# Kernel tuning notes

Measured on AMD Instinct MI355X. Metric: run time of the kernel, lower is better.

Reference implementation:

```python
import jax, jax.numpy as jnp
import numpy as np

# Static config (matches init_kwargs / input_specs)
B, P, A, D, K = 8, 1, 8, 8, 3          # batch, num_plans, action_channels, dim_qk, receptive_field
T, H, W = 32, 32, 32                   # 3D grid
PAD = K // 2
PA = P * A
PAD_VALUE = 0.0


def _pad3(t, val=PAD_VALUE):
    # pad last three (spatial) dims by PAD on each side
    return jnp.pad(t, ((0, 0), (0, 0), (PAD, PAD), (PAD, PAD), (PAD, PAD)), constant_values=val)


def _conv3d(x, w):
    # x: [B, Ci, T, H, W], w: [Co, Ci, K, K, K], VALID padding (input pre-padded)
    return jax.lax.conv_general_dilated(
        x, w, window_strides=(1, 1, 1), padding='VALID',
        dimension_numbers=('NCDHW', 'OIDHW', 'NCDHW'))


def setup_inputs() -> dict:
    key = jax.random.key(0)
    k1, k2, k3, k4 = jax.random.split(key, 4)
    s = 1.0 / np.sqrt(P * K ** 3)  # conv fan-in init scale
    return {
        'values':  jax.random.normal(k1, (B, P, T, H, W), jnp.float32),
        'rewards': jax.random.normal(k2, (B, P, T, H, W), jnp.float32),
        'w_qk':    jax.random.normal(k3, (2 * PA * D, P, K, K, K), jnp.float32) * s,
        'w_v':     jax.random.normal(k4, (PA, P, K, K, K), jnp.float32) * s,
    }


def reference(values, rewards, w_qk, w_v):
    x = values + rewards                       # [B, P, T, H, W]
    xp = _pad3(x)

    qk = _conv3d(xp, w_qk)                     # [B, 2*PA*D, T, H, W]
    q, k = jnp.split(qk, 2, axis=1)            # each [B, PA*D, T, H, W]

    # softmax value-conv weights over the flattened 3D kernel per (out, in) pair
    wv = jax.nn.softmax(w_v.reshape(PA, P, K ** 3), axis=-1).reshape(w_v.shape)
    v = _conv3d(xp, wv)                        # [B, PA, T, H, W]

    kp, vp = _pad3(k), _pad3(v)
    thw = T * H * W
    qf = q.reshape(B, PA, D, thw)              # [B, A, D, thw]

    # local 3x3x3 neighborhood attention: per kernel offset, dot q with shifted k
    # (same math as unfoldNd + einsum, without the K^3*D memory blow-up)
    sims, vns = [], []
    for dt in range(K):
        for dh in range(K):
            for dw in range(K):
                ksh = jax.lax.slice(kp, (0, 0, dt, dh, dw),
                                    (B, PA * D, dt + T, dh + H, dw + W)).reshape(B, PA, D, thw)
                sims.append(jnp.einsum('badt,badt->bat', qf, ksh))
                vns.append(jax.lax.slice(vp, (0, 0, dt, dh, dw),
                                         (B, PA, dt + T, dh + H, dw + W)).reshape(B, PA, thw))

    sim = jnp.stack(sims, axis=-1)             # [B, A, thw, K^3]
    attn = jax.nn.softmax(sim, axis=-1)
    vn = jnp.stack(vns, axis=2)                # [B, A, K^3, thw]
    q_values = jnp.einsum('batn,bant->bat', attn, vn)  # [B, A, thw]

    q_values = q_values.reshape(B, P, A, T, H, W)
    # ActionSelector with soft_maxpool=False: hard max over actions
    next_values = jnp.max(q_values, axis=2)    # [B, P, T, H, W]
    return next_values
```

## Files before the change

kernel.cpp:

```cpp
#include <hip/hip_runtime.h>
#include <hip/hip_bf16.h>

#define NB   8
#define NA   8
#define ND   8
#define NCH  64
#define GT   32
#define KREG 216
#define IMS  40

#define KACT_OFF 0
#define VP_OFF   27648
#define VSTR     592
#define QU_OFF   32384
#define POOL_SZ  40576

typedef _Float16 h2_t  __attribute__((ext_vector_type(2)));
typedef _Float16 f16x8 __attribute__((ext_vector_type(8)));
typedef float    f32x4 __attribute__((ext_vector_type(4)));

static __device__ __forceinline__ unsigned pack_h2(float a, float b) {
#if __has_builtin(__builtin_amdgcn_cvt_pkrtz)
    return __builtin_bit_cast(unsigned, __builtin_amdgcn_cvt_pkrtz(a, b));
#else
    unsigned short ha = __builtin_bit_cast(unsigned short, (_Float16)a);
    unsigned short hb = __builtin_bit_cast(unsigned short, (_Float16)b);
    return (unsigned)ha | ((unsigned)hb << 16);
#endif
}

static __device__ __forceinline__ float dot2(unsigned k, unsigned q, float c) {
#if __has_builtin(__builtin_amdgcn_fdot2)
    return __builtin_amdgcn_fdot2(__builtin_bit_cast(h2_t, k),
                                  __builtin_bit_cast(h2_t, q), c, false);
#else
    h2_t a = __builtin_bit_cast(h2_t, k), b = __builtin_bit_cast(h2_t, q);
    return c + (float)a[0] * (float)b[0] + (float)a[1] * (float)b[1];
#endif
}

__launch_bounds__(256, 4)
__global__ void avi_kernel(const float* __restrict__ values,
                           const float* __restrict__ rewards,
                           const float* __restrict__ w_qk,
                           const float* __restrict__ w_v,
                           float* __restrict__ out) {
    __shared__ __align__(16) char pool[POOL_SZ];
    float*    xS   = (float*)(pool + 0);
    _Float16* BTSl = (_Float16*)(pool + 2304);
    _Float16* imc  = (_Float16*)(pool + 13824);
    char*     qU   = pool + QU_OFF;

    const int tid  = threadIdx.x;
    const int bb   = blockIdx.x >> 9;
    const int tile = blockIdx.x & 511;
    const int tz = tile >> 6, ty = (tile >> 3) & 7, tx = tile & 7;
    const int g0z = tz * 4, g0y = ty * 4, g0x = tx * 4;
    const int base_in = bb * (GT * GT * GT);

    for (int i = tid; i < 512; i += 256) {
        int lz = i >> 6, ly = (i >> 3) & 7, lx = i & 7;
        int gz = g0z + lz - 2, gy = g0y + ly - 2, gx = g0x + lx - 2;
        float v = 0.f;
        if ((unsigned)gz < 32u && (unsigned)gy < 32u && (unsigned)gx < 32u) {
            int idx = base_in + gz * 1024 + gy * 32 + gx;
            v = values[idx] + rewards[idx];
        }
        xS[lz * 72 + ly * 9 + lx] = v;
    }
    if (tid < 144) {
        float r[28];
        r[27] = 0.f;
        if (tid < 64) {
            const float* w = w_qk + (NCH + tid) * 27;
            #pragma unroll
            for (int j = 0; j < 27; ++j) r[j] = w[j];
        } else if (tid < 72) {
            int a = tid - 64;
            float m = -1e30f;
            #pragma unroll
            for (int j = 0; j < 27; ++j) { r[j] = w_v[a * 27 + j]; m = fmaxf(m, r[j]); }
            float s = 0.f;
            #pragma unroll
            for (int j = 0; j < 27; ++j) { r[j] = __expf(r[j] - m); s += r[j]; }
            float inv = 1.f / s;
            #pragma unroll
            for (int j = 0; j < 27; ++j) r[j] *= inv;
        } else if (tid < 80) {
            #pragma unroll
            for (int j = 0; j < 27; ++j) r[j] = 0.f;
        } else {
            const float* w = w_qk + (tid - 80) * 27;
            const float L2E = 1.44269504f;
            #pragma unroll
            for (int j = 0; j < 27; ++j) r[j] = w[j] * L2E;
        }
        unsigned* dst = (unsigned*)(BTSl + tid * IMS);
        #pragma unroll
        for (int p = 0; p < 14; ++p) dst[p] = pack_h2(r[2 * p], r[2 * p + 1]);
        #pragma unroll
        for (int p = 14; p < 20; ++p) dst[p] = 0u;
    }
    __syncthreads();

    if (tid < 224) {
        unsigned rowU[16];
        if (tid < KREG) {
            int vz = tid / 36, rem = tid - vz * 36, vy = rem / 6, vx = rem - vy * 6;
            int gz = g0z + vz - 1, gy = g0y + vy - 1, gx = g0x + vx - 1;
            float mask = ((unsigned)gz < 32u && (unsigned)gy < 32u && (unsigned)gx < 32u)
                             ? 1.f : 0.f;
            float xr[27];
            #pragma unroll
            for (int t = 0; t < 27; ++t) {
                int dz = t / 9, dy = (t / 3) % 3, dx = t % 3;
                xr[t] = xS[(vz + dz) * 72 + (vy + dy) * 9 + (vx + dx)] * mask;
            }
            #pragma unroll
            for (int p = 0; p < 13; ++p) rowU[p] = pack_h2(xr[2 * p], xr[2 * p + 1]);
            rowU[13] = pack_h2(xr[26], 0.f);
            rowU[14] = rowU[15] = 0u;
        } else {
            #pragma unroll
            for (int p = 0; p < 16; ++p) rowU[p] = 0u;
        }
        int4* dst = (int4*)((char*)imc + tid * (IMS * 2));
        dst[0] = make_int4(rowU[0], rowU[1], rowU[2], rowU[3]);
        dst[1] = make_int4(rowU[4], rowU[5], rowU[6], rowU[7]);
        dst[2] = make_int4(rowU[8], rowU[9], rowU[10], rowU[11]);
        dst[3] = make_int4(rowU[12], rowU[13], rowU[14], rowU[15]);
    }

    const int lane = tid & 63;
    const int wave = tid >> 6;
    const int quad = lane >> 4;
    const int l15  = lane & 15;

    f16x8 af[9];
    #pragma unroll
    for (int mt = 0; mt < 9; ++mt)
        af[mt] = *(const f16x8*)(BTSl + (mt * 16 + l15) * IMS + quad * 8);

    __syncthreads();

    f16x8 bf[4];
    #pragma unroll
    for (int i = 0; i < 4; ++i) {
        int nt = wave + i * 4;
        if (nt < 14)
            bf[i] = *(const f16x8*)(imc + (nt * 16 + l15) * IMS + quad * 8);
    }

    __syncthreads();

    for (int i = 0; i < 4; ++i) {
        int nt = wave + i * 4;
        if (nt >= 14) break;
        int n = nt * 16 + l15;
        bool nvalid = (n < KREG);
        int vz = n / 36, rm = n - vz * 36, vy = rm / 6, vx = rm - vy * 6;
        bool ctr = ((unsigned)(vz - 1) < 4u) && ((unsigned)(vy - 1) < 4u) &&
                   ((unsigned)(vx - 1) < 4u);
        int cvox = (vz - 1) * 16 + (vy - 1) * 4 + (vx - 1);
        int kp_byte = (n * 16) ^ ((vz & 1) << 4);
        int qoff = cvox * 128 +
                   ((((quad >> 1) ^ (cvox >> 2) ^ (cvox & 3)) & 7) << 4) +
                   (quad & 1) * 8;
        #pragma unroll
        for (int mt = 0; mt < 9; ++mt) {
            f32x4 d = __builtin_amdgcn_mfma_f32_16x16x32_f16(
                af[mt], bf[i], (f32x4){0.f, 0.f, 0.f, 0.f}, 0, 0, 0);
            if (mt < 4) {
                if (nvalid) {
                    int a = mt * 2 + (quad >> 1);
                    int2 w2;
                    w2.x = (int)pack_h2(d[0], d[1]);
                    w2.y = (int)pack_h2(d[2], d[3]);
                    *(int2*)(pool + KACT_OFF + a * 3456 + kp_byte + (quad & 1) * 8) = w2;
                }
            } else if (mt == 4) {
                if (nvalid && quad < 2) {
                    #pragma unroll
                    for (int j = 0; j < 4; ++j)
                        *(_Float16*)(pool + VP_OFF + (quad * 4 + j) * VSTR +
                                     vz * 96 + vy * 16 + vx * 2) = (_Float16)d[j];
                }
            } else {
                if (ctr) {
                    int2 w2;
                    w2.x = (int)pack_h2(d[0], d[1]);
                    w2.y = (int)pack_h2(d[2], d[3]);
                    *(int2*)(qU + (qoff ^ ((mt - 5) << 5))) = w2;
                }
            }
        }
    }
    __syncthreads();

    const int a    = (tid >> 4) & 7;
    const int row  = tid & 15;
    const int h    = tid >> 7;
    const int clz2 = row >> 2, cly2 = row & 3;

    unsigned qp[4][4];
    {
        const char* qb = qU + row * 512;
        const int   u0 = (a ^ row) & 7;
        #pragma unroll
        for (int x = 0; x < 4; ++x) {
            const int4 qv = *(const int4*)(qb + x * 128 + ((u0 ^ x) << 4));
            qp[x][0] = (unsigned)qv.x; qp[x][1] = (unsigned)qv.y;
            qp[x][2] = (unsigned)qv.z; qp[x][3] = (unsigned)qv.w;
        }
    }

    float ssum[4] = {0.f, 0.f, 0.f, 0.f};
    float acc[4]  = {0.f, 0.f, 0.f, 0.f};

    const int   p   = clz2 & 1;
    const char* b0  = pool + KACT_OFF + a * 3456 + clz2 * 576 + cly2 * 96;
    const char* PAp = b0 + p * 16;
    const char* PBp = b0 + 16 - p * 16;
    const char* vb  = pool + VP_OFF + a * VSTR + clz2 * 96 + cly2 * 16;

#define STEP(PTA, PTB, KI, VI) do {                                           \
        int4 km[6];                                                           \
        km[0] = *(const int4*)((PTA) + (KI));                                 \
        km[1] = *(const int4*)((PTB) + (KI));                                 \
        km[2] = *(const int4*)((PTA) + (KI) + 32);                            \
        km[3] = *(const int4*)((PTB) + (KI) + 32);                            \
        km[4] = *(const int4*)((PTA) + (KI) + 64);                            \
        km[5] = *(const int4*)((PTB) + (KI) + 64);                            \
        f16x8 vv = *(const f16x8*)(vb + (VI));                                \
        float vf[6];                                                          \
        _Pragma("unroll")                                                     \
        for (int j = 0; j < 6; ++j) vf[j] = (float)vv[j];                     \
        _Pragma("unroll")                                                     \
        for (int x = 0; x < 4; ++x) {                                         \
            _Pragma("unroll")                                                 \
            for (int dx = 0; dx < 3; ++dx) {                                  \
                const int j = x + dx;                                         \
                float s = dot2((unsigned)km[j].x, qp[x][0],                   \
                          dot2((unsigned)km[j].y, qp[x][1],                   \
                          dot2((unsigned)km[j].z, qp[x][2],                   \
                          dot2((unsigned)km[j].w, qp[x][3], 0.f))));          \
                float e = exp2f(s);                                           \
                ssum[x] += e;                                                 \
                acc[x] = fmaf(e, vf[j], acc[x]);                              \
            }                                                                 \
        }                                                                     \
    } while (0)

#define HSTEP(PTA, PTB, KI, VI, X0) do {                                      \
        int4 km[4];                                                           \
        km[0] = *(const int4*)((PTA) + (KI) + (X0) * 16);                     \
        km[1] = *(const int4*)((PTB) + (KI) + (X0) * 16);                     \
        km[2] = *(const int4*)((PTA) + (KI) + (X0) * 16 + 32);                \
        km[3] = *(const int4*)((PTB) + (KI) + (X0) * 16 + 32);                \
        f16x8 vv = *(const f16x8*)(vb + (VI));                                \
        float vf[4];                                                          \
        _Pragma("unroll")                                                     \
        for (int j = 0; j < 4; ++j) vf[j] = (float)vv[(X0) + j];              \
        _Pragma("unroll")                                                     \
        for (int x = (X0); x < (X0) + 2; ++x) {                               \
            _Pragma("unroll")                                                 \
            for (int dx = 0; dx < 3; ++dx) {                                  \
                const int j = x + dx - (X0);                                  \
                float s = dot2((unsigned)km[j].x, qp[x][0],                   \
                          dot2((unsigned)km[j].y, qp[x][1],                   \
                          dot2((unsigned)km[j].z, qp[x][2],                   \
                          dot2((unsigned)km[j].w, qp[x][3], 0.f))));          \
                float e = exp2f(s);                                           \
                ssum[x] += e;                                                 \
                acc[x] = fmaf(e, vf[j], acc[x]);                              \
            }                                                                 \
        }                                                                     \
    } while (0)

    if (h == 0) {
        STEP(PAp, PBp, 0,    0);
        STEP(PAp, PBp, 96,   16);
        STEP(PAp, PBp, 192,  32);
        STEP(PBp, PAp, 576,  96);
        HSTEP(PBp, PAp, 672, 112, 0);
    } else {
        HSTEP(PBp, PAp, 672, 112, 2);
        STEP(PBp, PAp, 768,  128);
        STEP(PAp, PBp, 1152, 192);
        STEP(PAp, PBp, 1248, 208);
        STEP(PAp, PBp, 1344, 224);
    }
#undef STEP
#undef HSTEP

    float2* sc = (float2*)pool;
    __syncthreads();
    #pragma unroll
    for (int x = 0; x < 4; ++x)
        sc[(row * 4 + x) * 17 + a * 2 + h] = make_float2(ssum[x], acc[x]);
    __syncthreads();

    if (tid < 64) {
        float best = -1e30f;
        #pragma unroll
        for (int aa = 0; aa < 8; ++aa) {
            float2 p0 = sc[tid * 17 + aa * 2 + 0];
            float2 p1 = sc[tid * 17 + aa * 2 + 1];
            best = fmaxf(best, (p0.y + p1.y) / (p0.x + p1.x));
        }
        int lz2 = tid >> 4, ly2 = (tid >> 2) & 3, lx2 = tid & 3;
        int o = base_in + (g0z + lz2) * 1024 + (g0y + ly2) * 32 + (g0x + lx2);
        out[o] = best;
    }
}

extern "C" void kernel_launch(void* const* d_in, const int* in_sizes, int n_in,
                              void* d_out, int out_size, void* d_ws, size_t ws_size,
                              hipStream_t stream) {
    const float* values  = (const float*)d_in[0];
    const float* rewards = (const float*)d_in[1];
    const float* w_qk    = (const float*)d_in[2];
    const float* w_v     = (const float*)d_in[3];
    avi_kernel<<<NB * 512, 256, 0, stream>>>(values, rewards, w_qk, w_v,
                                             (float*)d_out);
}
```

Before: 102.5 us.

## Split fused conv+attention kernel into two kernels via workspace-staged q/k/v

Replaces the single fused kernel, which recomputed K and V over a halo region per tile in shared memory, with a conv kernel and an attention kernel. The conv kernel writes padded fp16 K, fp32 V and fp16 Q into global workspace, zeroing halo cells. The attention kernel then reads neighbour K/V from global memory with no halo recomputation and less shared memory, allowing higher occupancy. In exchange it adds roughly tens of MB of global traffic, a second launch, and a fallback to the old kernel when the workspace is too small.

```diff
diff --git a/kernel.cpp b/kernel.cpp
--- a/kernel.cpp
+++ b/kernel.cpp
@@ -9,11 +9,13 @@
 #define KREG 216
 #define IMS  40
 
-#define KACT_OFF 0
-#define VP_OFF   27648
-#define VSTR     592
-#define QU_OFF   32384
-#define POOL_SZ  40576
+#define KV_CELLS   39304
+#define KV_BYTES   (NB * KV_CELLS * 128)
+#define VP_WSOFF   KV_BYTES
+#define VP_BYTES   (NB * 8 * KV_CELLS * 4)
+#define QP_WSOFF   (VP_WSOFF + VP_BYTES)
+#define QP_BYTES   (NB * 32768 * 128)
+#define WS_NEED    (QP_WSOFF + QP_BYTES)
 
 typedef _Float16 h2_t  __attribute__((ext_vector_type(2)));
 typedef _Float16 f16x8 __attribute__((ext_vector_type(8)));
@@ -38,6 +40,226 @@
     return c + (float)a[0] * (float)b[0] + (float)a[1] * (float)b[1];
 #endif
 }
+
+static __device__ __forceinline__ float dot8(int4 k, const unsigned* q) {
+    return dot2((unsigned)k.x, q[0],
+           dot2((unsigned)k.y, q[1],
+           dot2((unsigned)k.z, q[2],
+           dot2((unsigned)k.w, q[3], 0.f))));
+}
+
+__launch_bounds__(256, 4)
+__global__ void conv_kernel(const float* __restrict__ values,
+                            const float* __restrict__ rewards,
+                            const float* __restrict__ w_qk,
+                            const float* __restrict__ w_v,
+                            _Float16* __restrict__ kvp,
+                            float* __restrict__ vp,
+                            _Float16* __restrict__ qp) {
+    __shared__ __align__(16) char pool[18944];
+    float*    xS   = (float*)(pool);
+    _Float16* BTSl = (_Float16*)(pool + 2304);
+    _Float16* imc  = (_Float16*)(pool + 13824);
+
+    const int tid  = threadIdx.x;
+    const int bb   = blockIdx.x >> 9;
+    const int tile = blockIdx.x & 511;
+    const int tz = tile >> 6, ty = (tile >> 3) & 7, tx = tile & 7;
+    const int g0z = tz * 4, g0y = ty * 4, g0x = tx * 4;
+    const int base_in = bb * 32768;
+
+    if (tid < KREG) {
+        int z = tid / 36, rem = tid - z * 36, y = rem / 6, x = rem - y * 6;
+        int gz = g0z + z - 1, gy = g0y + y - 1, gx = g0x + x - 1;
+        bool inb = ((unsigned)gz < 32u) && ((unsigned)gy < 32u) && ((unsigned)gx < 32u);
+        float v = 0.f;
+        if (inb) {
+            int idx = base_in + gz * 1024 + gy * 32 + gx;
+            v = values[idx] + rewards[idx];
+        }
+        xS[z * 72 + y * 9 + x] = v;
+        if (!inb) {
+            size_t cell = (size_t)(((gz + 1) * 34 + (gy + 1)) * 34 + (gx + 1));
+            int4* kr = (int4*)(kvp + ((size_t)bb * KV_CELLS + cell) * 64);
+            int4 z4 = make_int4(0, 0, 0, 0);
+            #pragma unroll
+            for (int p2 = 0; p2 < 8; ++p2) kr[p2] = z4;
+            #pragma unroll
+            for (int a2 = 0; a2 < 8; ++a2)
+                vp[((size_t)(bb * 8 + a2)) * KV_CELLS + cell] = 0.f;
+        }
+    }
+    if (tid < 144) {
+        float r[28];
+        r[27] = 0.f;
+        if (tid < 64) {
+            const float* w = w_qk + (NCH + tid) * 27;
+            #pragma unroll
+            for (int j = 0; j < 27; ++j) r[j] = w[j];
+        } else if (tid < 72) {
+            int a = tid - 64;
+            float m = -1e30f;
+            #pragma unroll
+            for (int j = 0; j < 27; ++j) { r[j] = w_v[a * 27 + j]; m = fmaxf(m, r[j]); }
+            float s = 0.f;
+            #pragma unroll
+            for (int j = 0; j < 27; ++j) { r[j] = __expf(r[j] - m); s += r[j]; }
+            float inv = 1.f / s;
+            #pragma unroll
+            for (int j = 0; j < 27; ++j) r[j] *= inv;
+        } else if (tid < 80) {
+            #pragma unroll
+            for (int j = 0; j < 27; ++j) r[j] = 0.f;
+        } else {
+            const float* w = w_qk + (tid - 80) * 27;
+            const float L2E = 1.44269504f;
+            #pragma unroll
+            for (int j = 0; j < 27; ++j) r[j] = w[j] * L2E;
+        }
+        unsigned* dst = (unsigned*)(BTSl + tid * IMS);
+        #pragma unroll
+        for (int p = 0; p < 14; ++p) dst[p] = pack_h2(r[2 * p], r[2 * p + 1]);
+        #pragma unroll
+        for (int p = 14; p < 20; ++p) dst[p] = 0u;
+    }
+    __syncthreads();
+
+    if (tid < 64) {
+        int cz = tid >> 4, cy = (tid >> 2) & 3, cx = tid & 3;
+        float xr[27];
+        #pragma unroll
+        for (int t = 0; t < 27; ++t) {
+            int dz = t / 9, dy = (t / 3) % 3, dx = t % 3;
+            xr[t] = xS[(cz + dz) * 72 + (cy + dy) * 9 + (cx + dx)];
+        }
+        unsigned rowU[16];
+        #pragma unroll
+        for (int p = 0; p < 13; ++p) rowU[p] = pack_h2(xr[2 * p], xr[2 * p + 1]);
+        rowU[13] = pack_h2(xr[26], 0.f);
+        rowU[14] = rowU[15] = 0u;
+        int4* dst = (int4*)((char*)imc + tid * (IMS * 2));
+        dst[0] = make_int4(rowU[0], rowU[1], rowU[2], rowU[3]);
+        dst[1] = make_int4(rowU[4], rowU[5], rowU[6], rowU[7]);
+        dst[2] = make_int4(rowU[8], rowU[9], rowU[10], rowU[11]);
+        dst[3] = make_int4(rowU[12], rowU[13], rowU[14], rowU[15]);
+    }
+    __syncthreads();
+
+    const int lane = tid & 63;
+    const int wave = tid >> 6;
+    const int quad = lane >> 4;
+    const int l15  = lane & 15;
+
+    f16x8 af[9];
+    #pragma unroll
+    for (int mt = 0; mt < 9; ++mt)
+        af[mt] = *(const f16x8*)(BTSl + (mt * 16 + l15) * IMS + quad * 8);
+    const f16x8 bfr = *(const f16x8*)(imc + (wave * 16 + l15) * IMS + quad * 8);
+
+    const int n  = wave * 16 + l15;
+    const int cz = n >> 4, cy = (n >> 2) & 3, cx = n & 3;
+    const size_t cellp = (size_t)(((g0z + cz + 1) * 34 + (g0y + cy + 1)) * 34 +
+                                  (g0x + cx + 1));
+    _Float16* krow = kvp + ((size_t)bb * KV_CELLS + cellp) * 64;
+    const int gvox = ((g0z + cz) * 32 + (g0y + cy)) * 32 + (g0x + cx);
+    _Float16* qrow = qp + ((size_t)base_in + gvox) * 64;
+
+    #pragma unroll
+    for (int mt = 0; mt < 9; ++mt) {
+        f32x4 d = __builtin_amdgcn_mfma_f32_16x16x32_f16(
+            af[mt], bfr, (f32x4){0.f, 0.f, 0.f, 0.f}, 0, 0, 0);
+        if (mt < 4) {
+            int ch0 = mt * 16 + quad * 4;
+            int2 w2;
+            w2.x = (int)pack_h2(d[0], d[1]);
+            w2.y = (int)pack_h2(d[2], d[3]);
+            *(int2*)(krow + ch0) = w2;
+        } else if (mt == 4) {
+            if (quad < 2) {
+                #pragma unroll
+                for (int j = 0; j < 4; ++j)
+                    vp[((size_t)(bb * 8 + quad * 4 + j)) * KV_CELLS + cellp] = d[j];
+            }
+        } else {
+            int ch0 = (mt - 5) * 16 + quad * 4;
+            int2 w2;
+            w2.x = (int)pack_h2(d[0], d[1]);
+            w2.y = (int)pack_h2(d[2], d[3]);
+            *(int2*)(qrow + ch0) = w2;
+        }
+    }
+}
+
+__launch_bounds__(256, 6)
+__global__ void attn_kernel(const _Float16* __restrict__ kvp,
+                            const float* __restrict__ vp,
+                            const _Float16* __restrict__ qp,
+                            float* __restrict__ out) {
+    __shared__ float sc[8][64];
+    const int tid = threadIdx.x;
+    const int swz  = (blockIdx.x & 7) * 512 + (blockIdx.x >> 3);
+    const int bb   = swz >> 9;
+    const int tile = swz & 511;
+    const int tz = tile >> 6, ty = (tile >> 3) & 7, tx = tile & 7;
+    const int g0z = tz * 4, g0y = ty * 4, g0x = tx * 4;
+
+    const int a   = tid >> 5;
+    const int run = tid & 31;
+    const int rz = run >> 3, ry = (run >> 1) & 3, x0 = (run & 1) * 2;
+
+    const int gvox = ((g0z + rz) * 32 + (g0y + ry)) * 32 + (g0x + x0);
+    const _Float16* q0 = qp + ((size_t)bb * 32768 + gvox) * 64 + a * 8;
+    const int4 qva = *(const int4*)(q0);
+    const int4 qvb = *(const int4*)(q0 + 64);
+    unsigned qA[4] = {(unsigned)qva.x, (unsigned)qva.y,
+                      (unsigned)qva.z, (unsigned)qva.w};
+    unsigned qB[4] = {(unsigned)qvb.x, (unsigned)qvb.y,
+                      (unsigned)qvb.z, (unsigned)qvb.w};
+
+    const size_t cell00 = (size_t)(((g0z + rz) * 34 + (g0y + ry)) * 34 +
+                                   (g0x + x0));
+    const _Float16* kb = kvp + ((size_t)bb * KV_CELLS + cell00) * 64 + a * 8;
+    const float*    vb = vp + ((size_t)(bb * 8 + a)) * KV_CELLS + cell00;
+
+    float ssA = 0.f, accA = 0.f, ssB = 0.f, accB = 0.f;
+    #pragma unroll
+    for (int dz = 0; dz < 3; ++dz) {
+        #pragma unroll
+        for (int dy = 0; dy < 3; ++dy) {
+            const int off = (dz * 34 + dy) * 34;
+            const _Float16* kr = kb + (size_t)off * 64;
+            const int4 k0 = *(const int4*)(kr);
+            const int4 k1 = *(const int4*)(kr + 64);
+            const int4 k2 = *(const int4*)(kr + 128);
+            const int4 k3 = *(const int4*)(kr + 192);
+            const float2 v01 = *(const float2*)(vb + off);
+            const float2 v23 = *(const float2*)(vb + off + 2);
+            float e;
+            e = exp2f(dot8(k0, qA)); ssA += e; accA = fmaf(e, v01.x, accA);
+            e = exp2f(dot8(k1, qA)); ssA += e; accA = fmaf(e, v01.y, accA);
+            e = exp2f(dot8(k2, qA)); ssA += e; accA = fmaf(e, v23.x, accA);
+            e = exp2f(dot8(k1, qB)); ssB += e; accB = fmaf(e, v01.y, accB);
+            e = exp2f(dot8(k2, qB)); ssB += e; accB = fmaf(e, v23.x, accB);
+            e = exp2f(dot8(k3, qB)); ssB += e; accB = fmaf(e, v23.y, accB);
+        }
+    }
+    *(float2*)&sc[a][run * 2] = make_float2(accA / ssA, accB / ssB);
+    __syncthreads();
+
+    if (tid < 64) {
+        float best = -1e30f;
+        #pragma unroll
+        for (int aa = 0; aa < 8; ++aa) best = fmaxf(best, sc[aa][tid]);
+        int z = tid >> 4, y = (tid >> 2) & 3, x = tid & 3;
+        out[bb * 32768 + ((g0z + z) * 32 + (g0y + y)) * 32 + (g0x + x)] = best;
+    }
+}
+
+#define KACT_OFF 0
+#define VP_OFF   27648
+#define VSTR     592
+#define QU_OFF   32384
+#define POOL_SZ  40576
 
 __launch_bounds__(256, 4)
 __global__ void avi_kernel(const float* __restrict__ values,
@@ -293,19 +515,19 @@
 #undef STEP
 #undef HSTEP
 
-    float2* sc = (float2*)pool;
+    float2* sc2 = (float2*)pool;
     __syncthreads();
     #pragma unroll
     for (int x = 0; x < 4; ++x)
-        sc[(row * 4 + x) * 17 + a * 2 + h] = make_float2(ssum[x], acc[x]);
+        sc2[(row * 4 + x) * 17 + a * 2 + h] = make_float2(ssum[x], acc[x]);
     __syncthreads();
 
     if (tid < 64) {
         float best = -1e30f;
         #pragma unroll
         for (int aa = 0; aa < 8; ++aa) {
-            float2 p0 = sc[tid * 17 + aa * 2 + 0];
-            float2 p1 = sc[tid * 17 + aa * 2 + 1];
+            float2 p0 = sc2[tid * 17 + aa * 2 + 0];
+            float2 p1 = sc2[tid * 17 + aa * 2 + 1];
             best = fmaxf(best, (p0.y + p1.y) / (p0.x + p1.x));
         }
         int lz2 = tid >> 4, ly2 = (tid >> 2) & 3, lx2 = tid & 3;
@@ -321,6 +543,15 @@
     const float* rewards = (const float*)d_in[1];
     const float* w_qk    = (const float*)d_in[2];
     const float* w_v     = (const float*)d_in[3];
-    avi_kernel<<<NB * 512, 256, 0, stream>>>(values, rewards, w_qk, w_v,
-                                             (float*)d_out);
-}
+    if (ws_size >= (size_t)WS_NEED && d_ws != nullptr) {
+        _Float16* kvp = (_Float16*)d_ws;
+        float*    vp  = (float*)((char*)d_ws + VP_WSOFF);
+        _Float16* qp  = (_Float16*)((char*)d_ws + QP_WSOFF);
+        conv_kernel<<<NB * 512, 256, 0, stream>>>(values, rewards, w_qk, w_v,
+                                                  kvp, vp, qp);
+        attn_kernel<<<NB * 512, 256, 0, stream>>>(kvp, vp, qp, (float*)d_out);
+    } else {
+        avi_kernel<<<NB * 512, 256, 0, stream>>>(values, rewards, w_qk, w_v,
+                                                 (float*)d_out);
+    }
+}
```

Measured after the change: 196.4 us. +91.5%, slower.

## Double threads per block and split attention x-columns across thread halves

Applied to the files above, without the earlier changes.

Launches 512 threads per tile instead of 256, so each thread in the attention phase handles two x-voxels instead of four. The MFMA projection phase distributes its n-tiles across eight waves. The goal is to cut per-thread serial work and register pressure and to increase latency hiding. In exchange, barriers span larger blocks and some K loads are duplicated across the thread halves.

```diff
diff --git a/kernel.cpp b/kernel.cpp
--- a/kernel.cpp
+++ b/kernel.cpp
@@ -16,6 +16,7 @@
 #define POOL_SZ  40576
 
 typedef _Float16 h2_t  __attribute__((ext_vector_type(2)));
+typedef _Float16 f16x4 __attribute__((ext_vector_type(4)));
 typedef _Float16 f16x8 __attribute__((ext_vector_type(8)));
 typedef float    f32x4 __attribute__((ext_vector_type(4)));
 
@@ -39,7 +40,7 @@
 #endif
 }
 
-__launch_bounds__(256, 4)
+__launch_bounds__(512, 8)
 __global__ void avi_kernel(const float* __restrict__ values,
                            const float* __restrict__ rewards,
                            const float* __restrict__ w_qk,
@@ -58,8 +59,8 @@
     const int g0z = tz * 4, g0y = ty * 4, g0x = tx * 4;
     const int base_in = bb * (GT * GT * GT);
 
-    for (int i = tid; i < 512; i += 256) {
-        int lz = i >> 6, ly = (i >> 3) & 7, lx = i & 7;
+    {
+        int lz = tid >> 6, ly = (tid >> 3) & 7, lx = tid & 7;
         int gz = g0z + lz - 2, gy = g0y + ly - 2, gx = g0x + lx - 2;
         float v = 0.f;
         if ((unsigned)gz < 32u && (unsigned)gy < 32u && (unsigned)gx < 32u) {
@@ -143,18 +144,18 @@
 
     __syncthreads();
 
-    f16x8 bf[4];
+    f16x8 bf[2];
     #pragma unroll
-    for (int i = 0; i < 4; ++i) {
-        int nt = wave + i * 4;
+    for (int i = 0; i < 2; ++i) {
+        int nt = wave + i * 8;
         if (nt < 14)
             bf[i] = *(const f16x8*)(imc + (nt * 16 + l15) * IMS + quad * 8);
     }
 
     __syncthreads();
 
-    for (int i = 0; i < 4; ++i) {
-        int nt = wave + i * 4;
+    for (int i = 0; i < 2; ++i) {
+        int nt = wave + i * 8;
         if (nt >= 14) break;
         int n = nt * 16 + l15;
         bool nvalid = (n < KREG);
@@ -197,107 +198,108 @@
     }
     __syncthreads();
 
-    const int a    = (tid >> 4) & 7;
     const int row  = tid & 15;
-    const int h    = tid >> 7;
+    const int xh   = (tid >> 4) & 1;
+    const int a    = (tid >> 5) & 7;
+    const int h    = tid >> 8;
     const int clz2 = row >> 2, cly2 = row & 3;
-
-    unsigned qp[4][4];
+    const int X0   = xh * 2;
+
+    unsigned qp[2][4];
     {
         const char* qb = qU + row * 512;
         const int   u0 = (a ^ row) & 7;
         #pragma unroll
-        for (int x = 0; x < 4; ++x) {
+        for (int xl = 0; xl < 2; ++xl) {
+            int x = X0 + xl;
             const int4 qv = *(const int4*)(qb + x * 128 + ((u0 ^ x) << 4));
-            qp[x][0] = (unsigned)qv.x; qp[x][1] = (unsigned)qv.y;
-            qp[x][2] = (unsigned)qv.z; qp[x][3] = (unsigned)qv.w;
-        }
-    }
-
-    float ssum[4] = {0.f, 0.f, 0.f, 0.f};
-    float acc[4]  = {0.f, 0.f, 0.f, 0.f};
+            qp[xl][0] = (unsigned)qv.x; qp[xl][1] = (unsigned)qv.y;
+            qp[xl][2] = (unsigned)qv.z; qp[xl][3] = (unsigned)qv.w;
+        }
+    }
+
+    float ssum[2] = {0.f, 0.f};
+    float acc[2]  = {0.f, 0.f};
 
     const int   p   = clz2 & 1;
     const char* b0  = pool + KACT_OFF + a * 3456 + clz2 * 576 + cly2 * 96;
-    const char* PAp = b0 + p * 16;
-    const char* PBp = b0 + 16 - p * 16;
-    const char* vb  = pool + VP_OFF + a * VSTR + clz2 * 96 + cly2 * 16;
-
-#define STEP(PTA, PTB, KI, VI) do {                                           \
-        int4 km[6];                                                           \
+    const char* PAx = b0 + p * 16 + X0 * 16;
+    const char* PBx = b0 + 16 - p * 16 + X0 * 16;
+    const char* vb  = pool + VP_OFF + a * VSTR + clz2 * 96 + cly2 * 16 + X0 * 2;
+
+#define STEP2(PTA, PTB, KI, VI) do {                                          \
+        int4 km[4];                                                           \
         km[0] = *(const int4*)((PTA) + (KI));                                 \
         km[1] = *(const int4*)((PTB) + (KI));                                 \
         km[2] = *(const int4*)((PTA) + (KI) + 32);                            \
         km[3] = *(const int4*)((PTB) + (KI) + 32);                            \
-        km[4] = *(const int4*)((PTA) + (KI) + 64);                            \
-        km[5] = *(const int4*)((PTB) + (KI) + 64);                            \
-        f16x8 vv = *(const f16x8*)(vb + (VI));                                \
-        float vf[6];                                                          \
+        f16x4 vv = *(const f16x4*)(vb + (VI));                                \
+        float vf[4];                                                          \
         _Pragma("unroll")                                                     \
-        for (int j = 0; j < 6; ++j) vf[j] = (float)vv[j];                     \
+        for (int j = 0; j < 4; ++j) vf[j] = (float)vv[j];                     \
         _Pragma("unroll")                                                     \
-        for (int x = 0; x < 4; ++x) {                                         \
+        for (int xl = 0; xl < 2; ++xl) {                                      \
             _Pragma("unroll")                                                 \
             for (int dx = 0; dx < 3; ++dx) {                                  \
-                const int j = x + dx;                                         \
-                float s = dot2((unsigned)km[j].x, qp[x][0],                   \
-                          dot2((unsigned)km[j].y, qp[x][1],                   \
-                          dot2((unsigned)km[j].z, qp[x][2],                   \
-                          dot2((unsigned)km[j].w, qp[x][3], 0.f))));          \
+                const int j = xl + dx;                                        \
+                float s = dot2((unsigned)km[j].x, qp[xl][0],                  \
+                          dot2((unsigned)km[j].y, qp[xl][1],                  \
+                          dot2((unsigned)km[j].z, qp[xl][2],                  \
+                          dot2((unsigned)km[j].w, qp[xl][3], 0.f))));         \
                 float e = exp2f(s);                                           \
-                ssum[x] += e;                                                 \
-                acc[x] = fmaf(e, vf[j], acc[x]);                              \
+                ssum[xl] += e;                                                \
+                acc[xl] = fmaf(e, vf[j], acc[xl]);                            \
             }                                                                 \
         }                                                                     \
     } while (0)
 
-#define HSTEP(PTA, PTB, KI, VI, X0) do {                                      \
-        int4 km[4];                                                           \
-        km[0] = *(const int4*)((PTA) + (KI) + (X0) * 16);                     \
-        km[1] = *(const int4*)((PTB) + (KI) + (X0) * 16);                     \
-        km[2] = *(const int4*)((PTA) + (KI) + (X0) * 16 + 32);                \
-        km[3] = *(const int4*)((PTB) + (KI) + (X0) * 16 + 32);                \
-        f16x8 vv = *(const f16x8*)(vb + (VI));                                \
-        float vf[4];                                                          \
+#define QSTEP(PTA, PTB, KI, VI, XL) do {                                      \
+        int4 km[3];                                                           \
+        if ((XL) == 0) {                                                      \
+            km[0] = *(const int4*)((PTA) + (KI));                             \
+            km[1] = *(const int4*)((PTB) + (KI));                             \
+            km[2] = *(const int4*)((PTA) + (KI) + 32);                        \
+        } else {                                                              \
+            km[0] = *(const int4*)((PTB) + (KI));                             \
+            km[1] = *(const int4*)((PTA) + (KI) + 32);                        \
+            km[2] = *(const int4*)((PTB) + (KI) + 32);                        \
+        }                                                                     \
+        f16x4 vv = *(const f16x4*)(vb + (VI));                                \
         _Pragma("unroll")                                                     \
-        for (int j = 0; j < 4; ++j) vf[j] = (float)vv[(X0) + j];              \
-        _Pragma("unroll")                                                     \
-        for (int x = (X0); x < (X0) + 2; ++x) {                               \
-            _Pragma("unroll")                                                 \
-            for (int dx = 0; dx < 3; ++dx) {                                  \
-                const int j = x + dx - (X0);                                  \
-                float s = dot2((unsigned)km[j].x, qp[x][0],                   \
-                          dot2((unsigned)km[j].y, qp[x][1],                   \
-                          dot2((unsigned)km[j].z, qp[x][2],                   \
-                          dot2((unsigned)km[j].w, qp[x][3], 0.f))));          \
-                float e = exp2f(s);                                           \
-                ssum[x] += e;                                                 \
-                acc[x] = fmaf(e, vf[j], acc[x]);                              \
-            }                                                                 \
+        for (int dx = 0; dx < 3; ++dx) {                                      \
+            float s = dot2((unsigned)km[dx].x, qp[XL][0],                     \
+                      dot2((unsigned)km[dx].y, qp[XL][1],                     \
+                      dot2((unsigned)km[dx].z, qp[XL][2],                     \
+                      dot2((unsigned)km[dx].w, qp[XL][3], 0.f))));            \
+            float e = exp2f(s);                                               \
+            ssum[XL] += e;                                                    \
+            acc[XL] = fmaf(e, (float)vv[(XL) + dx], acc[XL]);                 \
         }                                                                     \
     } while (0)
 
     if (h == 0) {
-        STEP(PAp, PBp, 0,    0);
-        STEP(PAp, PBp, 96,   16);
-        STEP(PAp, PBp, 192,  32);
-        STEP(PBp, PAp, 576,  96);
-        HSTEP(PBp, PAp, 672, 112, 0);
+        STEP2(PAx, PBx, 0,    0);
+        STEP2(PAx, PBx, 96,   16);
+        STEP2(PAx, PBx, 192,  32);
+        STEP2(PBx, PAx, 576,  96);
+        QSTEP(PBx, PAx, 672, 112, 0);
     } else {
-        HSTEP(PBp, PAp, 672, 112, 2);
-        STEP(PBp, PAp, 768,  128);
-        STEP(PAp, PBp, 1152, 192);
-        STEP(PAp, PBp, 1248, 208);
-        STEP(PAp, PBp, 1344, 224);
-    }
-#undef STEP
-#undef HSTEP
+        QSTEP(PBx, PAx, 672, 112, 1);
+        STEP2(PBx, PAx, 768,  128);
+        STEP2(PAx, PBx, 1152, 192);
+        STEP2(PAx, PBx, 1248, 208);
+        STEP2(PAx, PBx, 1344, 224);
+    }
+#undef STEP2
+#undef QSTEP
 
     float2* sc = (float2*)pool;
     __syncthreads();
     #pragma unroll
-    for (int x = 0; x < 4; ++x)
-        sc[(row * 4 + x) * 17 + a * 2 + h] = make_float2(ssum[x], acc[x]);
+    for (int xl = 0; xl < 2; ++xl) {
+        int vox = row * 4 + X0 + xl;
+        sc[vox * 17 + a * 2 + h] = make_float2(ssum[xl], acc[xl]);
+    }
     __syncthreads();
 
     if (tid < 64) {
@@ -321,6 +323,6 @@
     const float* rewards = (const float*)d_in[1];
     const float* w_qk    = (const float*)d_in[2];
     const float* w_v     = (const float*)d_in[3];
-    avi_kernel<<<NB * 512, 256, 0, stream>>>(values, rewards, w_qk, w_v,
+    avi_kernel<<<NB * 512, 512, 0, stream>>>(values, rewards, w_qk, w_v,
                                              (float*)d_out);
 }
```

Measured after the change: 105.9 us. 3.2% more time.
